# Kernel optimization log

Measured on AMD Instinct MI355X. Metric: run time of the kernel, lower is better.

## Reference

```python
import jax, jax.numpy as jnp
import numpy as np

F_IN, F_OUT, H, L_ENC, L_DEC, HORIZON = 32, 8, 64, 2, 2, 48
B, T = 2048, 512


def _lstm_cell(x, h, c, Wih, Whh, bih, bhh):
    # PyTorch LSTMCell: gates ordered i, f, g, o
    g = x @ Wih.T + bih + h @ Whh.T + bhh
    i, f, gg, o = jnp.split(g, 4, axis=-1)
    c_new = jax.nn.sigmoid(f) * c + jax.nn.sigmoid(i) * jnp.tanh(gg)
    h_new = jax.nn.sigmoid(o) * jnp.tanh(c_new)
    return h_new, c_new


def setup_inputs() -> dict:
    key = jax.random.key(0)
    ks = jax.random.split(key, 16)
    s = 1.0 / np.sqrt(H)
    u = lambda k, shape: jax.random.uniform(k, shape, jnp.float32, -s, s)
    return {
        "X": jax.random.normal(ks[0], (B, T, F_IN), jnp.float32),
        "X_mask": jnp.ones((B, T, F_IN), jnp.float32),
        "W_emb": u(ks[1], (H, F_IN)),
        "b_emb": u(ks[2], (H,)),
        "enc_Wih": u(ks[3], (L_ENC, 4 * H, H)),
        "enc_Whh": u(ks[4], (L_ENC, 4 * H, H)),
        "enc_bih": u(ks[5], (L_ENC, 4 * H)),
        "enc_bhh": u(ks[6], (L_ENC, 4 * H)),
        "dec_Wih": u(ks[7], (L_DEC, 4 * H, H)),
        "dec_Whh": u(ks[8], (L_DEC, 4 * H, H)),
        "dec_bih": u(ks[9], (L_DEC, 4 * H)),
        "dec_bhh": u(ks[10], (L_DEC, 4 * H)),
        "W_reg": u(ks[11], (F_OUT, H)),
        "b_reg": u(ks[12], (F_OUT,)),
    }


def reference(X, X_mask, W_emb, b_emb, enc_Wih, enc_Whh, enc_bih, enc_bhh,
              dec_Wih, dec_Whh, dec_bih, dec_bhh, W_reg, b_reg):
    batch = X.shape[0]
    # Token embedding for all timesteps at once: [T, B, H]
    emb = jnp.einsum('btf,hf->tbh', X, W_emb) + b_emb

    h0 = jnp.zeros((L_ENC, batch, H), X.dtype)
    c0 = jnp.zeros((L_ENC, batch, H), X.dtype)

    def enc_step(carry, x_t):
        h, c = carry
        h_t = x_t
        hs, cs = [], []
        for i in range(L_ENC):
            h_t, c_t = _lstm_cell(h_t, h[i], c[i], enc_Wih[i], enc_Whh[i], enc_bih[i], enc_bhh[i])
            hs.append(h_t)
            cs.append(c_t)
        return (jnp.stack(hs), jnp.stack(cs)), None

    (h_enc, _), _ = jax.lax.scan(enc_step, (h0, c0), emb)

    # Decoder: hidden states initialized from encoder h, cells from zero
    c_dec0 = jnp.zeros((L_DEC, batch, H), X.dtype)

    def dec_step(carry, _):
        h, c = carry
        h_t = h[-1]
        hs, cs = [], []
        for i in range(L_DEC):
            h_t, c_t = _lstm_cell(h_t, h[i], c[i], dec_Wih[i], dec_Whh[i], dec_bih[i], dec_bhh[i])
            hs.append(h_t)
            cs.append(c_t)
        y_t = h_t @ W_reg.T + b_reg
        return (jnp.stack(hs), jnp.stack(cs)), y_t

    _, ys = jax.lax.scan(dec_step, (h_enc, c_dec0), None, length=HORIZON)
    return jnp.transpose(ys, (1, 0, 2))  # [B, horizon, F_OUT]
```

## Files before the change

### kernel.cpp

```cpp
#include <hip/hip_runtime.h>
#include <hip/hip_bf16.h>

typedef __bf16 bf16x8 __attribute__((ext_vector_type(8)));
typedef float  f32x4  __attribute__((ext_vector_type(4)));

#define MFMA16(a,b,c) __builtin_amdgcn_mfma_f32_16x16x32_bf16((a),(b),(c),0,0,0)

__device__ __forceinline__ bf16x8 cvt8(f32x4 a, f32x4 b){
  bf16x8 r;
  r[0]=(__bf16)a[0]; r[1]=(__bf16)a[1]; r[2]=(__bf16)a[2]; r[3]=(__bf16)a[3];
  r[4]=(__bf16)b[0]; r[5]=(__bf16)b[1]; r[6]=(__bf16)b[2]; r[7]=(__bf16)b[3];
  return r;
}
__device__ __forceinline__ bf16x8 ld8(const float* p){
  return cvt8(*(const f32x4*)p, *(const f32x4*)(p+4));
}
__device__ __forceinline__ float sigm(float x){
  return __builtin_amdgcn_rcpf(1.f + __expf(-x));
}
__device__ __forceinline__ float tanhx(float x){
  return 1.f - 2.f*__builtin_amdgcn_rcpf(1.f + __expf(2.f*x));
}
__device__ __forceinline__ float sel4(const f32x4& v, int q){
  float ab = (q&1) ? v[1] : v[0];
  float cd = (q&1) ? v[3] : v[2];
  return (q&2) ? cd : ab;
}

struct Acc4 { f32x4 a[4]; };

__device__ __forceinline__ Acc4 gates_mfma(const __bf16 (*XH)[144],
                                           const bf16x8 wfl[4][4],
                                           const float gbl[4],
                                           int row, int quad){
  bf16x8 afr[4];
#pragma unroll
  for (int ks=0; ks<4; ++ks)
    afr[ks] = *(const bf16x8*)&XH[row][ks*32 + quad*8];
  Acc4 A;
#pragma unroll
  for (int g=0; g<4; ++g){ float bb = gbl[g]; A.a[g] = (f32x4){bb,bb,bb,bb}; }
#pragma unroll
  for (int ks=0; ks<4; ++ks)
#pragma unroll
    for (int g=0; g<4; ++g)
      A.a[g] = MFMA16(afr[ks], wfl[g][ks], A.a[g]);
  return A;
}

extern "C" __global__ void __launch_bounds__(256, 2)
seq2seq_kernel(const float* __restrict__ X,
               const float* __restrict__ Wemb, const float* __restrict__ bemb,
               const float* __restrict__ eWih, const float* __restrict__ eWhh,
               const float* __restrict__ ebih, const float* __restrict__ ebhh,
               const float* __restrict__ dWih, const float* __restrict__ dWhh,
               const float* __restrict__ dbih, const float* __restrict__ dbhh,
               const float* __restrict__ Wreg, const float* __restrict__ breg,
               float* __restrict__ out)
{
  __shared__ __align__(16) __bf16 XH0[4][144];
  __shared__ __align__(16) __bf16 XH1[4][144];

  const int tid  = (int)threadIdx.x;
  const int wg   = tid >> 6;
  const int lane = tid & 63;
  const int col  = lane & 15;
  const int row  = col & 3;
  const int quad = lane >> 4;
  const int u    = wg*16 + col;
  const int b0   = (int)blockIdx.x * 4;
  const int brow = b0 + row;

  for (int i = tid; i < 4*144; i += 256){
    (&XH0[0][0])[i] = (__bf16)0.f;
    (&XH1[0][0])[i] = (__bf16)0.f;
  }

  bf16x8 wembf = ld8(Wemb + u*32 + quad*8);
  const float eb = bemb[u];

  bf16x8 wr[2];
#pragma unroll
  for (int ks=0; ks<2; ++ks) wr[ks] = ld8(Wreg + (col&7)*64 + ks*32 + quad*8);
  const float rb = breg[col&7];

  bf16x8 wf[2][4][4];
  float  gb[2][4];
#pragma unroll
  for (int l=0; l<2; ++l){
#pragma unroll
    for (int g=0; g<4; ++g){
      const int n = g*64 + u;
      gb[l][g] = ebih[l*256+n] + ebhh[l*256+n];
#pragma unroll
      for (int ks=0; ks<4; ++ks){
        const float* srcw = (ks < 2) ? eWih : eWhh;
        wf[l][g][ks] = ld8(srcw + ((size_t)(l*256+n))*64 + (ks&1)*32 + quad*8);
      }
    }
  }

  float c0 = 0.f, c1 = 0.f;
  const float* xb = X + (size_t)brow*512*32 + quad*8;
  f32x4 pa[2], pb[2];

  __syncthreads();

  {
    f32x4 xa = *(const f32x4*)xb, xv = *(const f32x4*)(xb+4);
    pa[1] = *(const f32x4*)(xb+32); pb[1] = *(const f32x4*)(xb+36);
    pa[0] = *(const f32x4*)(xb+64); pb[0] = *(const f32x4*)(xb+68);
    f32x4 ea = (f32x4){eb,eb,eb,eb};
    ea = MFMA16(cvt8(xa,xv), wembf, ea);
    XH0[quad][u] = (__bf16)sel4(ea, quad);
  }
  __syncthreads();

#pragma unroll 2
  for (int t=0; t<512; ++t){
    Acc4 A = gates_mfma(XH0, wf[0], gb[0], row, quad);
    float gi = sigm (sel4(A.a[0], quad));
    float gf = sigm (sel4(A.a[1], quad));
    float gg = tanhx(sel4(A.a[2], quad));
    float go = sigm (sel4(A.a[3], quad));
    c0 = gf*c0 + gi*gg;
    __bf16 hb = (__bf16)(go * tanhx(c0));
    __syncthreads();
    {
      const int s = (t+1)&1;
      f32x4 ea = (f32x4){eb,eb,eb,eb};
      ea = MFMA16(cvt8(pa[s],pb[s]), wembf, ea);
      int tn = t+3; if (tn > 511) tn = 511;
      pa[s] = *(const f32x4*)(xb + (size_t)tn*32);
      pb[s] = *(const f32x4*)(xb + (size_t)tn*32 + 4);
      XH0[quad][u] = (__bf16)sel4(ea, quad);
    }
    XH0[quad][64+u] = hb;
    XH1[quad][u]    = hb;
    __syncthreads();
    A = gates_mfma(XH1, wf[1], gb[1], row, quad);
    gi = sigm (sel4(A.a[0], quad));
    gf = sigm (sel4(A.a[1], quad));
    gg = tanhx(sel4(A.a[2], quad));
    go = sigm (sel4(A.a[3], quad));
    c1 = gf*c1 + gi*gg;
    hb = (__bf16)(go * tanhx(c1));
    __syncthreads();
    XH1[quad][64+u] = hb;
  }
  __syncthreads();

  if (tid < 256){
    int r = tid >> 6, cc = tid & 63;
    XH0[r][cc] = XH1[r][64 + cc];
  }

#pragma unroll
  for (int l=0; l<2; ++l){
#pragma unroll
    for (int g=0; g<4; ++g){
      const int n = g*64 + u;
      gb[l][g] = dbih[l*256+n] + dbhh[l*256+n];
#pragma unroll
      for (int ks=0; ks<4; ++ks){
        const float* srcw = (ks < 2) ? dWih : dWhh;
        wf[l][g][ks] = ld8(srcw + ((size_t)(l*256+n))*64 + (ks&1)*32 + quad*8);
      }
    }
  }
  c0 = 0.f; c1 = 0.f;
  __syncthreads();

  for (int t=0; t<48; ++t){
    Acc4 A = gates_mfma(XH0, wf[0], gb[0], row, quad);
    float gi = sigm (sel4(A.a[0], quad));
    float gf = sigm (sel4(A.a[1], quad));
    float gg = tanhx(sel4(A.a[2], quad));
    float go = sigm (sel4(A.a[3], quad));
    c0 = gf*c0 + gi*gg;
    __bf16 hb = (__bf16)(go * tanhx(c0));
    __syncthreads();
    XH0[quad][64+u] = hb;
    XH1[quad][u]    = hb;
    __syncthreads();
    A = gates_mfma(XH1, wf[1], gb[1], row, quad);
    gi = sigm (sel4(A.a[0], quad));
    gf = sigm (sel4(A.a[1], quad));
    gg = tanhx(sel4(A.a[2], quad));
    go = sigm (sel4(A.a[3], quad));
    c1 = gf*c1 + gi*gg;
    hb = (__bf16)(go * tanhx(c1));
    __syncthreads();
    XH1[quad][64+u] = hb;
    XH0[quad][u]    = hb;
    __syncthreads();
    f32x4 ya = (f32x4){rb,rb,rb,rb};
#pragma unroll
    for (int ks=0; ks<2; ++ks){
      bf16x8 ah = *(const bf16x8*)&XH1[row][64 + ks*32 + quad*8];
      ya = MFMA16(ah, wr[ks], ya);
    }
    if (wg == 0 && quad == 0 && col < 8){
#pragma unroll
      for (int r=0; r<4; ++r)
        out[((size_t)(b0 + r)*48 + t)*8 + col] = ya[r];
    }
  }
}

extern "C" void kernel_launch(void* const* d_in, const int* in_sizes, int n_in,
                              void* d_out, int out_size, void* d_ws, size_t ws_size,
                              hipStream_t stream)
{
  (void)in_sizes; (void)n_in; (void)out_size; (void)d_ws; (void)ws_size;
  const float* X    = (const float*)d_in[0];
  const float* Wemb = (const float*)d_in[2];
  const float* bemb = (const float*)d_in[3];
  const float* eWih = (const float*)d_in[4];
  const float* eWhh = (const float*)d_in[5];
  const float* ebih = (const float*)d_in[6];
  const float* ebhh = (const float*)d_in[7];
  const float* dWih = (const float*)d_in[8];
  const float* dWhh = (const float*)d_in[9];
  const float* dbih = (const float*)d_in[10];
  const float* dbhh = (const float*)d_in[11];
  const float* Wreg = (const float*)d_in[12];
  const float* breg = (const float*)d_in[13];
  float* out = (float*)d_out;

  seq2seq_kernel<<<dim3(512), dim3(256), 0, stream>>>(
      X, Wemb, bemb, eWih, eWhh, ebih, ebhh,
      dWih, dWhh, dbih, dbhh, Wreg, breg, out);
}
```

Baseline: 721.3 us.

## Process 8 batch rows per 512-thread block with gate exchange through shared memory

Each block now handles 8 batch rows with 8 waves instead of 4 rows with 4 waves. Each wave computes 32 gate columns across all gates by MFMA. The gate pre-activations go to shared-memory G buffers, and the elementwise LSTM update is then done with one thread per (row, unit). This uses more MFMA rows per tile (8 of 16 instead of 4) and halves the grid to 256 blocks. The cost is an extra barrier and an LDS round-trip per layer step, plus fewer blocks than the 256 CUs can overlap, which lengthens the serial chain per step.

```diff
diff --git a/kernel.cpp b/kernel.cpp
--- a/kernel.cpp
+++ b/kernel.cpp
@@ -21,34 +21,8 @@
 __device__ __forceinline__ float tanhx(float x){
   return 1.f - 2.f*__builtin_amdgcn_rcpf(1.f + __expf(2.f*x));
 }
-__device__ __forceinline__ float sel4(const f32x4& v, int q){
-  float ab = (q&1) ? v[1] : v[0];
-  float cd = (q&1) ? v[3] : v[2];
-  return (q&2) ? cd : ab;
-}
-
-struct Acc4 { f32x4 a[4]; };
-
-__device__ __forceinline__ Acc4 gates_mfma(const __bf16 (*XH)[144],
-                                           const bf16x8 wfl[4][4],
-                                           const float gbl[4],
-                                           int row, int quad){
-  bf16x8 afr[4];
-#pragma unroll
-  for (int ks=0; ks<4; ++ks)
-    afr[ks] = *(const bf16x8*)&XH[row][ks*32 + quad*8];
-  Acc4 A;
-#pragma unroll
-  for (int g=0; g<4; ++g){ float bb = gbl[g]; A.a[g] = (f32x4){bb,bb,bb,bb}; }
-#pragma unroll
-  for (int ks=0; ks<4; ++ks)
-#pragma unroll
-    for (int g=0; g<4; ++g)
-      A.a[g] = MFMA16(afr[ks], wfl[g][ks], A.a[g]);
-  return A;
-}
-
-extern "C" __global__ void __launch_bounds__(256, 2)
+
+extern "C" __global__ void __launch_bounds__(512, 1)
 seq2seq_kernel(const float* __restrict__ X,
                const float* __restrict__ Wemb, const float* __restrict__ bemb,
                const float* __restrict__ eWih, const float* __restrict__ eWhh,
@@ -58,44 +32,49 @@
                const float* __restrict__ Wreg, const float* __restrict__ breg,
                float* __restrict__ out)
 {
-  __shared__ __align__(16) __bf16 XH0[4][144];
-  __shared__ __align__(16) __bf16 XH1[4][144];
+  __shared__ __align__(16) __bf16 XH0[8][144];
+  __shared__ __align__(16) __bf16 XH1[8][144];
+  __shared__ __align__(16) float G0[8][264];
+  __shared__ __align__(16) float G1[8][264];
 
   const int tid  = (int)threadIdx.x;
-  const int wg   = tid >> 6;
+  const int w    = tid >> 6;
   const int lane = tid & 63;
   const int col  = lane & 15;
-  const int row  = col & 3;
   const int quad = lane >> 4;
-  const int u    = wg*16 + col;
-  const int b0   = (int)blockIdx.x * 4;
-  const int brow = b0 + row;
-
-  for (int i = tid; i < 4*144; i += 256){
+  const int row8 = col & 7;
+  const int b0   = (int)blockIdx.x * 8;
+  const int brow = b0 + row8;
+
+  for (int i = tid; i < 8*144; i += 512){
     (&XH0[0][0])[i] = (__bf16)0.f;
     (&XH1[0][0])[i] = (__bf16)0.f;
   }
 
-  bf16x8 wembf = ld8(Wemb + u*32 + quad*8);
-  const float eb = bemb[u];
+  const int n0 = 32*w + col;
+  const int n1 = n0 + 16;
+
+  const int ue = (w&3)*16 + col;
+  bf16x8 wembf = ld8(Wemb + ue*32 + quad*8);
+  const float eb = bemb[ue];
 
   bf16x8 wr[2];
 #pragma unroll
   for (int ks=0; ks<2; ++ks) wr[ks] = ld8(Wreg + (col&7)*64 + ks*32 + quad*8);
   const float rb = breg[col&7];
 
-  bf16x8 wf[2][4][4];
-  float  gb[2][4];
+  bf16x8 wf[2][2][4];
+  float  gbias[2][2];
 #pragma unroll
   for (int l=0; l<2; ++l){
 #pragma unroll
-    for (int g=0; g<4; ++g){
-      const int n = g*64 + u;
-      gb[l][g] = ebih[l*256+n] + ebhh[l*256+n];
+    for (int ti=0; ti<2; ++ti){
+      const int n = ti ? n1 : n0;
+      gbias[l][ti] = ebih[l*256+n] + ebhh[l*256+n];
 #pragma unroll
       for (int ks=0; ks<4; ++ks){
         const float* srcw = (ks < 2) ? eWih : eWhh;
-        wf[l][g][ks] = ld8(srcw + ((size_t)(l*256+n))*64 + (ks&1)*32 + quad*8);
+        wf[l][ti][ks] = ld8(srcw + ((size_t)(l*256+n))*64 + (ks&1)*32 + quad*8);
       }
     }
   }
@@ -106,65 +85,105 @@
 
   __syncthreads();
 
-  {
+  if (w < 4){
     f32x4 xa = *(const f32x4*)xb, xv = *(const f32x4*)(xb+4);
     pa[1] = *(const f32x4*)(xb+32); pb[1] = *(const f32x4*)(xb+36);
     pa[0] = *(const f32x4*)(xb+64); pb[0] = *(const f32x4*)(xb+68);
     f32x4 ea = (f32x4){eb,eb,eb,eb};
     ea = MFMA16(cvt8(xa,xv), wembf, ea);
-    XH0[quad][u] = (__bf16)sel4(ea, quad);
+    if (quad < 2){
+#pragma unroll
+      for (int r=0; r<4; ++r) XH0[quad*4+r][ue] = (__bf16)ea[r];
+    }
   }
   __syncthreads();
 
 #pragma unroll 2
   for (int t=0; t<512; ++t){
-    Acc4 A = gates_mfma(XH0, wf[0], gb[0], row, quad);
-    float gi = sigm (sel4(A.a[0], quad));
-    float gf = sigm (sel4(A.a[1], quad));
-    float gg = tanhx(sel4(A.a[2], quad));
-    float go = sigm (sel4(A.a[3], quad));
-    c0 = gf*c0 + gi*gg;
-    __bf16 hb = (__bf16)(go * tanhx(c0));
-    __syncthreads();
-    {
-      const int s = (t+1)&1;
-      f32x4 ea = (f32x4){eb,eb,eb,eb};
-      ea = MFMA16(cvt8(pa[s],pb[s]), wembf, ea);
-      int tn = t+3; if (tn > 511) tn = 511;
-      pa[s] = *(const f32x4*)(xb + (size_t)tn*32);
-      pb[s] = *(const f32x4*)(xb + (size_t)tn*32 + 4);
-      XH0[quad][u] = (__bf16)sel4(ea, quad);
-    }
-    XH0[quad][64+u] = hb;
-    XH1[quad][u]    = hb;
-    __syncthreads();
-    A = gates_mfma(XH1, wf[1], gb[1], row, quad);
-    gi = sigm (sel4(A.a[0], quad));
-    gf = sigm (sel4(A.a[1], quad));
-    gg = tanhx(sel4(A.a[2], quad));
-    go = sigm (sel4(A.a[3], quad));
-    c1 = gf*c1 + gi*gg;
-    hb = (__bf16)(go * tanhx(c1));
-    __syncthreads();
-    XH1[quad][64+u] = hb;
-  }
-  __syncthreads();
-
-  if (tid < 256){
+    {
+      bf16x8 afr[4];
+#pragma unroll
+      for (int ks=0; ks<4; ++ks)
+        afr[ks] = *(const bf16x8*)&XH0[row8][ks*32 + quad*8];
+      f32x4 a0 = (f32x4){gbias[0][0],gbias[0][0],gbias[0][0],gbias[0][0]};
+      f32x4 a1 = (f32x4){gbias[0][1],gbias[0][1],gbias[0][1],gbias[0][1]};
+#pragma unroll
+      for (int ks=0; ks<4; ++ks){
+        a0 = MFMA16(afr[ks], wf[0][0][ks], a0);
+        a1 = MFMA16(afr[ks], wf[0][1][ks], a1);
+      }
+      if (quad < 2){
+#pragma unroll
+        for (int r=0; r<4; ++r){ G0[quad*4+r][n0] = a0[r]; G0[quad*4+r][n1] = a1[r]; }
+      }
+    }
+    __syncthreads();
+    {
+      float gi = sigm (G0[w][lane]);
+      float gf = sigm (G0[w][64+lane]);
+      float gg = tanhx(G0[w][128+lane]);
+      float go = sigm (G0[w][192+lane]);
+      c0 = gf*c0 + gi*gg;
+      __bf16 hb = (__bf16)(go * tanhx(c0));
+      XH0[w][64+lane] = hb;
+      XH1[w][lane]    = hb;
+      if (w < 4){
+        const int s = (t+1)&1;
+        f32x4 ea = (f32x4){eb,eb,eb,eb};
+        ea = MFMA16(cvt8(pa[s],pb[s]), wembf, ea);
+        int tn = t+3; if (tn > 511) tn = 511;
+        pa[s] = *(const f32x4*)(xb + (size_t)tn*32);
+        pb[s] = *(const f32x4*)(xb + (size_t)tn*32 + 4);
+        if (quad < 2){
+#pragma unroll
+          for (int r=0; r<4; ++r) XH0[quad*4+r][ue] = (__bf16)ea[r];
+        }
+      }
+    }
+    __syncthreads();
+    {
+      bf16x8 afr[4];
+#pragma unroll
+      for (int ks=0; ks<4; ++ks)
+        afr[ks] = *(const bf16x8*)&XH1[row8][ks*32 + quad*8];
+      f32x4 a0 = (f32x4){gbias[1][0],gbias[1][0],gbias[1][0],gbias[1][0]};
+      f32x4 a1 = (f32x4){gbias[1][1],gbias[1][1],gbias[1][1],gbias[1][1]};
+#pragma unroll
+      for (int ks=0; ks<4; ++ks){
+        a0 = MFMA16(afr[ks], wf[1][0][ks], a0);
+        a1 = MFMA16(afr[ks], wf[1][1][ks], a1);
+      }
+      if (quad < 2){
+#pragma unroll
+        for (int r=0; r<4; ++r){ G1[quad*4+r][n0] = a0[r]; G1[quad*4+r][n1] = a1[r]; }
+      }
+    }
+    __syncthreads();
+    {
+      float gi = sigm (G1[w][lane]);
+      float gf = sigm (G1[w][64+lane]);
+      float gg = tanhx(G1[w][128+lane]);
+      float go = sigm (G1[w][192+lane]);
+      c1 = gf*c1 + gi*gg;
+      XH1[w][64+lane] = (__bf16)(go * tanhx(c1));
+    }
+  }
+  __syncthreads();
+
+  {
     int r = tid >> 6, cc = tid & 63;
     XH0[r][cc] = XH1[r][64 + cc];
   }
-
 #pragma unroll
   for (int l=0; l<2; ++l){
 #pragma unroll
-    for (int g=0; g<4; ++g){
-      const int n = g*64 + u;
-      gb[l][g] = dbih[l*256+n] + dbhh[l*256+n];
+    for (int ti=0; ti<2; ++ti){
+      const int n = ti ? n1 : n0;
+      gbias[l][ti] = dbih[l*256+n] + dbhh[l*256+n];
 #pragma unroll
       for (int ks=0; ks<4; ++ks){
         const float* srcw = (ks < 2) ? dWih : dWhh;
-        wf[l][g][ks] = ld8(srcw + ((size_t)(l*256+n))*64 + (ks&1)*32 + quad*8);
+        wf[l][ti][ks] = ld8(srcw + ((size_t)(l*256+n))*64 + (ks&1)*32 + quad*8);
       }
     }
   }
@@ -172,38 +191,76 @@
   __syncthreads();
 
   for (int t=0; t<48; ++t){
-    Acc4 A = gates_mfma(XH0, wf[0], gb[0], row, quad);
-    float gi = sigm (sel4(A.a[0], quad));
-    float gf = sigm (sel4(A.a[1], quad));
-    float gg = tanhx(sel4(A.a[2], quad));
-    float go = sigm (sel4(A.a[3], quad));
-    c0 = gf*c0 + gi*gg;
-    __bf16 hb = (__bf16)(go * tanhx(c0));
-    __syncthreads();
-    XH0[quad][64+u] = hb;
-    XH1[quad][u]    = hb;
-    __syncthreads();
-    A = gates_mfma(XH1, wf[1], gb[1], row, quad);
-    gi = sigm (sel4(A.a[0], quad));
-    gf = sigm (sel4(A.a[1], quad));
-    gg = tanhx(sel4(A.a[2], quad));
-    go = sigm (sel4(A.a[3], quad));
-    c1 = gf*c1 + gi*gg;
-    hb = (__bf16)(go * tanhx(c1));
-    __syncthreads();
-    XH1[quad][64+u] = hb;
-    XH0[quad][u]    = hb;
-    __syncthreads();
-    f32x4 ya = (f32x4){rb,rb,rb,rb};
-#pragma unroll
-    for (int ks=0; ks<2; ++ks){
-      bf16x8 ah = *(const bf16x8*)&XH1[row][64 + ks*32 + quad*8];
-      ya = MFMA16(ah, wr[ks], ya);
-    }
-    if (wg == 0 && quad == 0 && col < 8){
-#pragma unroll
-      for (int r=0; r<4; ++r)
-        out[((size_t)(b0 + r)*48 + t)*8 + col] = ya[r];
+    {
+      bf16x8 afr[4];
+#pragma unroll
+      for (int ks=0; ks<4; ++ks)
+        afr[ks] = *(const bf16x8*)&XH0[row8][ks*32 + quad*8];
+      f32x4 a0 = (f32x4){gbias[0][0],gbias[0][0],gbias[0][0],gbias[0][0]};
+      f32x4 a1 = (f32x4){gbias[0][1],gbias[0][1],gbias[0][1],gbias[0][1]};
+#pragma unroll
+      for (int ks=0; ks<4; ++ks){
+        a0 = MFMA16(afr[ks], wf[0][0][ks], a0);
+        a1 = MFMA16(afr[ks], wf[0][1][ks], a1);
+      }
+      if (quad < 2){
+#pragma unroll
+        for (int r=0; r<4; ++r){ G0[quad*4+r][n0] = a0[r]; G0[quad*4+r][n1] = a1[r]; }
+      }
+    }
+    __syncthreads();
+    {
+      float gi = sigm (G0[w][lane]);
+      float gf = sigm (G0[w][64+lane]);
+      float gg = tanhx(G0[w][128+lane]);
+      float go = sigm (G0[w][192+lane]);
+      c0 = gf*c0 + gi*gg;
+      __bf16 hb = (__bf16)(go * tanhx(c0));
+      XH0[w][64+lane] = hb;
+      XH1[w][lane]    = hb;
+    }
+    __syncthreads();
+    {
+      bf16x8 afr[4];
+#pragma unroll
+      for (int ks=0; ks<4; ++ks)
+        afr[ks] = *(const bf16x8*)&XH1[row8][ks*32 + quad*8];
+      f32x4 a0 = (f32x4){gbias[1][0],gbias[1][0],gbias[1][0],gbias[1][0]};
+      f32x4 a1 = (f32x4){gbias[1][1],gbias[1][1],gbias[1][1],gbias[1][1]};
+#pragma unroll
+      for (int ks=0; ks<4; ++ks){
+        a0 = MFMA16(afr[ks], wf[1][0][ks], a0);
+        a1 = MFMA16(afr[ks], wf[1][1][ks], a1);
+      }
+      if (quad < 2){
+#pragma unroll
+        for (int r=0; r<4; ++r){ G1[quad*4+r][n0] = a0[r]; G1[quad*4+r][n1] = a1[r]; }
+      }
+    }
+    __syncthreads();
+    {
+      float gi = sigm (G1[w][lane]);
+      float gf = sigm (G1[w][64+lane]);
+      float gg = tanhx(G1[w][128+lane]);
+      float go = sigm (G1[w][192+lane]);
+      c1 = gf*c1 + gi*gg;
+      __bf16 hb = (__bf16)(go * tanhx(c1));
+      XH1[w][64+lane] = hb;
+      XH0[w][lane]    = hb;
+    }
+    __syncthreads();
+    if (w == 0){
+      f32x4 ya = (f32x4){rb,rb,rb,rb};
+#pragma unroll
+      for (int ks=0; ks<2; ++ks){
+        bf16x8 ah = *(const bf16x8*)&XH1[row8][64 + ks*32 + quad*8];
+        ya = MFMA16(ah, wr[ks], ya);
+      }
+      if (quad < 2 && col < 8){
+#pragma unroll
+        for (int r=0; r<4; ++r)
+          out[((size_t)(b0 + quad*4 + r)*48 + t)*8 + col] = ya[r];
+      }
     }
   }
 }
@@ -228,7 +285,7 @@
   const float* breg = (const float*)d_in[13];
   float* out = (float*)d_out;
 
-  seq2seq_kernel<<<dim3(512), dim3(256), 0, stream>>>(
+  seq2seq_kernel<<<dim3(256), dim3(512), 0, stream>>>(
       X, Wemb, bemb, eWih, eWhh, ebih, ebhh,
       dWih, dWhh, dbih, dbhh, Wreg, breg, out);
 }
```

Result: slower. 776.2 us (+7.6%).
